# Kernel tuning notes

Measured on AMD Instinct MI355X. Metric: run time of the kernel, lower is better.

The kernel has to match this reference:

```python
import jax, jax.numpy as jnp
import numpy as np

N, L = 16, 1024
VOCAB = 32000
D_EMB = 512
D_HID = 512
N_LAYER = 2
N_CLASS = 64
NEG_INF = -1.0e9


def setup_inputs() -> dict:
    key = jax.random.key(0)
    ks = jax.random.split(key, 12)
    s = 0.02
    return {
        "x": jax.random.randint(ks[0], (N, L), 0, VOCAB),
        "eos": jax.random.randint(ks[1], (N,), 0, L),
        "emb": jax.random.normal(ks[2], (VOCAB, D_EMB), jnp.float32) * s,
        # stacked RNN weights: layer 0 input is D_EMB == D_HID so stacking is valid
        "W_ih": jax.random.normal(ks[3], (N_LAYER, D_HID, D_HID), jnp.float32) * s,
        "W_hh": jax.random.normal(ks[4], (N_LAYER, D_HID, D_HID), jnp.float32) * s,
        "b_ih": jax.random.normal(ks[5], (N_LAYER, D_HID), jnp.float32) * s,
        "b_hh": jax.random.normal(ks[6], (N_LAYER, D_HID), jnp.float32) * s,
        "Wc": jax.random.normal(ks[7], (D_HID, 2 * D_HID), jnp.float32) * s,
        "bc": jax.random.normal(ks[8], (D_HID,), jnp.float32) * s,
        "Wd": jax.random.normal(ks[9], (N_CLASS, D_HID), jnp.float32) * s,
        "bd": jax.random.normal(ks[10], (N_CLASS,), jnp.float32) * s,
    }


def _rnn(inp, W_ih, W_hh, b_ih, b_hh):
    # inp: (N, L, D); stacked tanh Elman RNN, batch_first
    out = inp
    for l in range(N_LAYER):
        Wi, Wh = W_ih[l], W_hh[l]
        b = b_ih[l] + b_hh[l]
        xs = jnp.einsum('nld,hd->lnh', out, Wi) + b  # precompute input proj, (L,N,H)
        def step(h, xt):
            h = jnp.tanh(xt + h @ Wh.T)
            return h, h
        h0 = jnp.zeros((out.shape[0], D_HID), out.dtype)
        _, ys = jax.lax.scan(step, h0, xs)  # (L, N, H)
        out = ys.transpose(1, 0, 2)
    return out


def _attention(out):
    # scores[b,t,s] = <out[b,t], out[b,s]>; strict-causal mask as in the torch code:
    # tril(scores, -1) + triu(-1e9) (diagonal and above get -1e9)
    scores = jnp.einsum('bld,bmd->blm', out, out)
    Lm = scores.shape[-1]
    masked = jnp.tril(scores, -1) + jnp.triu(jnp.full((Lm, Lm), NEG_INF, scores.dtype))
    att = jax.nn.softmax(masked, axis=-1)
    att_vec = jnp.einsum('blm,bmd->bld', att, out)
    return att_vec, att


def reference(x, eos, emb, W_ih, W_hh, b_ih, b_hh, Wc, bc, Wd, bd):
    h = emb[x]                                   # (N, L, D_EMB)
    out = _rnn(h, W_ih, W_hh, b_ih, b_hh)        # (N, L, D_HID)
    att_vec, att_scores = _attention(out)
    # one-hot(eos) matmul == gather at eos position
    idx = jnp.arange(out.shape[0])
    z = out[idx, eos]                            # (N, D_HID)
    att_z = att_vec[idx, eos]                    # (N, D_HID)
    dec_in = jnp.concatenate([att_z, z], axis=-1) @ Wc.T + bc
    logit = dec_in @ Wd.T + bd                   # (N, N_CLASS)
    return logit
```

## Files before the change

### kernel.cpp

```cpp
#include <hip/hip_runtime.h>
#include <cmath>

#define NB   16
#define LL   1024
#define DD   512
#define NCLS 64

__global__ __launch_bounds__(256) void k_gemm_embed(
    const int* __restrict__ x, const float* __restrict__ emb,
    const float* __restrict__ W, const float* __restrict__ b1,
    const float* __restrict__ b2, float* __restrict__ C)
{
  __shared__ __align__(16) float As[16][132];
  __shared__ __align__(16) float Ws[16][132];
  const int tid = threadIdx.x;
  const int n0 = (blockIdx.x & 3) * 128;
  const int m0 = (blockIdx.x >> 2) * 128;
  const int tm = tid & 15, tn = tid >> 4;
  float acc[8][8] = {};

  const int r = tid >> 1;
  const int q = (tid & 1) * 2;
  const long arow = (long)x[m0 + r] * DD;
  const long wrow = (long)(n0 + r) * DD;

  float4 a0 = *(const float4*)(emb + arow + q * 4);
  float4 a1 = *(const float4*)(emb + arow + q * 4 + 4);
  float4 w0 = *(const float4*)(W + wrow + q * 4);
  float4 w1 = *(const float4*)(W + wrow + q * 4 + 4);

  for (int k0 = 0; k0 < DD; k0 += 16) {
    __syncthreads();
    As[q*4+0][r]=a0.x; As[q*4+1][r]=a0.y; As[q*4+2][r]=a0.z; As[q*4+3][r]=a0.w;
    As[q*4+4][r]=a1.x; As[q*4+5][r]=a1.y; As[q*4+6][r]=a1.z; As[q*4+7][r]=a1.w;
    Ws[q*4+0][r]=w0.x; Ws[q*4+1][r]=w0.y; Ws[q*4+2][r]=w0.z; Ws[q*4+3][r]=w0.w;
    Ws[q*4+4][r]=w1.x; Ws[q*4+5][r]=w1.y; Ws[q*4+6][r]=w1.z; Ws[q*4+7][r]=w1.w;
    if (k0 + 16 < DD) {
      a0 = *(const float4*)(emb + arow + k0 + 16 + q * 4);
      a1 = *(const float4*)(emb + arow + k0 + 16 + q * 4 + 4);
      w0 = *(const float4*)(W + wrow + k0 + 16 + q * 4);
      w1 = *(const float4*)(W + wrow + k0 + 16 + q * 4 + 4);
    }
    __syncthreads();
    #pragma unroll
    for (int kk = 0; kk < 16; ++kk) {
      float4 aL = *(const float4*)&As[kk][tm * 4];
      float4 aH = *(const float4*)&As[kk][64 + tm * 4];
      float4 wL = *(const float4*)&Ws[kk][tn * 4];
      float4 wH = *(const float4*)&Ws[kk][64 + tn * 4];
      const float av[8] = {aL.x,aL.y,aL.z,aL.w, aH.x,aH.y,aH.z,aH.w};
      const float wv[8] = {wL.x,wL.y,wL.z,wL.w, wH.x,wH.y,wH.z,wH.w};
      #pragma unroll
      for (int i = 0; i < 8; ++i)
        #pragma unroll
        for (int j = 0; j < 8; ++j)
          acc[i][j] += av[i] * wv[j];
    }
  }
  float bj[8];
  #pragma unroll
  for (int j = 0; j < 8; ++j) {
    const int c = n0 + ((j < 4) ? tn * 4 + j : 64 + tn * 4 + (j - 4));
    bj[j] = b1[c] + b2[c];
  }
  #pragma unroll
  for (int i = 0; i < 8; ++i) {
    const int m = m0 + ((i < 4) ? tm * 4 + i : 64 + tm * 4 + (i - 4));
    float4 o1 = { acc[i][0]+bj[0], acc[i][1]+bj[1], acc[i][2]+bj[2], acc[i][3]+bj[3] };
    float4 o2 = { acc[i][4]+bj[4], acc[i][5]+bj[5], acc[i][6]+bj[6], acc[i][7]+bj[7] };
    *(float4*)(C + (long)m * DD + n0 + tn * 4)      = o1;
    *(float4*)(C + (long)m * DD + n0 + 64 + tn * 4) = o2;
  }
}

template<int CTRL>
__device__ __forceinline__ float dpp_add(float x) {
  int s = __builtin_amdgcn_update_dpp(0, __float_as_int(x), CTRL, 0xF, 0xF, true);
  return x + __int_as_float(s);
}
__device__ __forceinline__ float wave_red8(float y) {
  y = dpp_add<0xB1>(y);
  y = dpp_add<0x4E>(y);
  y = dpp_add<0x141>(y);
  return y;
}

__device__ __forceinline__ float fast_tanh(float x) {
  float e = __expf(2.0f * x);
  return 1.0f - __fdividef(2.0f, 1.0f + e);
}

__device__ __forceinline__ float poll_ld(const float* p) {
  return __hip_atomic_load(p, __ATOMIC_RELAXED, __HIP_MEMORY_SCOPE_AGENT);
}
__device__ __forceinline__ void enc_st(float* p, float v) {
  __hip_atomic_store(p, v + 2.0f, __ATOMIC_RELAXED, __HIP_MEMORY_SCOPE_AGENT);
}
__device__ __forceinline__ void st_drain() {
  asm volatile("s_waitcnt vmcnt(0)" ::: "memory");
}
__device__ __forceinline__ void dot64(const float* w, const float4* h4, float4& a) {
  #pragma unroll
  for (int q = 0; q < 16; ++q) {
    float4 h = h4[q];
    a.x += w[4*q+0]*h.x; a.y += w[4*q+1]*h.y;
    a.z += w[4*q+2]*h.z; a.w += w[4*q+3]*h.w;
  }
}
__device__ __forceinline__ float hsum4(const float4& a) { return (a.x+a.y)+(a.z+a.w); }

__global__ __launch_bounds__(256, 2) void k_scan(
    const float* __restrict__ W_ih, const float* __restrict__ W_hh,
    const float* __restrict__ b_ih, const float* __restrict__ b_hh,
    float* __restrict__ Bbuf,
    float* __restrict__ Abuf)
{
  const int g = blockIdx.x;
  const int lay = g >> 8;
  const int b = g & 15;
  const int j = (g & 255) >> 4;
  const int tid = threadIdx.x;
  const int part = tid & 7;
  const int rl  = tid >> 3;
  const int row = j * 32 + rl;
  const bool leader = (part == 0);

  __shared__ __align__(16) float hS[2][8 * 68];
  __shared__ __align__(16) float hT[2][8 * 68];

  float* Bb = Bbuf + (long)b * LL * DD;
  float* Ab = Abuf + (long)b * LL * DD;

  const int i0 = tid, i1 = tid + 256;
  const int d0 = (i0 >> 6) * 68 + (i0 & 63);
  const int d1 = (i1 >> 6) * 68 + (i1 & 63);

  if (lay == 0) {
    float w1[64];
    {
      const float* p1 = W_hh + (long)row * DD + part * 64;
      #pragma unroll
      for (int q = 0; q < 64; ++q) w1[q] = p1[q];
    }
    #pragma unroll
    for (int q = 0; q < 64; ++q) asm volatile("" : "+v"(w1[q]));

    float xpv = 0.f, xnext = 0.f;
    if (leader) {
      xpv   = Bb[row];
      xnext = Bb[DD + row];
      enc_st(Bb + row, fast_tanh(xpv));
    }
    st_drain();
    for (int t = 1; t < LL; ++t) {
      const int bufi = t & 1;
      xpv = xnext;
      if (leader && (t + 1 < LL)) xnext = Bb[(long)(t + 1) * DD + row];
      const float* s1 = Bb + (long)(t - 1) * DD;
      float v0 = poll_ld(s1 + i0), v1 = poll_ld(s1 + i1);
      while (fminf(v0, v1) <= 1.0f) {
        __builtin_amdgcn_s_sleep(2);
        v0 = poll_ld(s1 + i0); v1 = poll_ld(s1 + i1);
      }
      hS[bufi][d0] = v0 - 2.0f; hS[bufi][d1] = v1 - 2.0f;
      __syncthreads();
      float4 a = {0.f, 0.f, 0.f, 0.f};
      dot64(w1, (const float4*)&hS[bufi][part * 68], a);
      float y = wave_red8(hsum4(a));
      if (leader) enc_st(Bb + (long)t * DD + row, fast_tanh(xpv + y));
      st_drain();
    }
  } else {
    float w2[64], w3[64];
    {
      const float* p2 = W_ih + (long)DD * DD + (long)row * DD + part * 64;
      const float* p3 = W_hh + (long)DD * DD + (long)row * DD + part * 64;
      #pragma unroll
      for (int q = 0; q < 64; ++q) { w2[q] = p2[q]; w3[q] = p3[q]; }
    }
    #pragma unroll
    for (int q = 0; q < 64; ++q) {
      asm volatile("" : "+v"(w2[q]));
      asm volatile("" : "+v"(w3[q]));
    }
    const float bias2 = b_ih[DD + row] + b_hh[DD + row];

    float xin2;
    {
      const float* s1 = Bb;
      float v0 = poll_ld(s1 + i0), v1 = poll_ld(s1 + i1);
      while (fminf(v0, v1) <= 1.0f) {
        __builtin_amdgcn_s_sleep(2);
        v0 = poll_ld(s1 + i0); v1 = poll_ld(s1 + i1);
      }
      hT[1][d0] = v0 - 2.0f; hT[1][d1] = v1 - 2.0f;
      __syncthreads();
      float4 a = {0.f, 0.f, 0.f, 0.f};
      dot64(w2, (const float4*)&hT[1][part * 68], a);
      xin2 = wave_red8(hsum4(a)) + bias2;
    }
    for (int t = 0; t < LL; ++t) {
      const int bufi = t & 1;
      const bool st2 = (t >= 1);
      const bool st1 = (t + 1 < LL);
      {
        const float* s2 = Ab + (long)(t - 1) * DD;
        const float* s1 = Bb + (long)(t + 1) * DD;
        float u0 = 3.f, u1 = 3.f, v0 = 3.f, v1 = 3.f;
        if (st2) { u0 = poll_ld(s2 + i0); u1 = poll_ld(s2 + i1); }
        if (st1) { v0 = poll_ld(s1 + i0); v1 = poll_ld(s1 + i1); }
        while (fminf(fminf(u0, u1), fminf(v0, v1)) <= 1.0f) {
          __builtin_amdgcn_s_sleep(2);
          if (st2) { u0 = poll_ld(s2 + i0); u1 = poll_ld(s2 + i1); }
          if (st1) { v0 = poll_ld(s1 + i0); v1 = poll_ld(s1 + i1); }
        }
        if (st2) { hS[bufi][d0] = u0 - 2.0f; hS[bufi][d1] = u1 - 2.0f; }
        if (st1) { hT[bufi][d0] = v0 - 2.0f; hT[bufi][d1] = v1 - 2.0f; }
      }
      __syncthreads();
      float y3 = 0.f;
      if (st2) {
        float4 a = {0.f, 0.f, 0.f, 0.f};
        dot64(w3, (const float4*)&hS[bufi][part * 68], a);
        y3 = hsum4(a);
      }
      y3 = wave_red8(y3);
      if (leader) enc_st(Ab + (long)t * DD + row, fast_tanh(xin2 + y3));
      st_drain();
      if (st1) {
        float4 a = {0.f, 0.f, 0.f, 0.f};
        dot64(w2, (const float4*)&hT[bufi][part * 68], a);
        xin2 = wave_red8(hsum4(a)) + bias2;
      }
    }
  }
}

__global__ __launch_bounds__(256) void k_attn(
    const float* __restrict__ O2, const int* __restrict__ eos,
    const float* __restrict__ Wc, const float* __restrict__ bc,
    const float* __restrict__ Wd, const float* __restrict__ bd,
    float* __restrict__ out)
{
  const int b = blockIdx.x;
  const int tid = threadIdx.x;
  const int te = eos[b];
  __shared__ __align__(16) float q[DD];
  __shared__ float ps[LL];
  __shared__ float red[256];
  __shared__ __align__(16) float din[2 * DD];
  __shared__ __align__(16) float dvec[DD];
  const float* Ob = O2 + (long)b * LL * DD;
  const float4* Ob4 = (const float4*)Ob;

  float qpart = 0.f;
  for (int i = tid; i < DD; i += 256) {
    float v = Ob[(long)te * DD + i] - 2.0f;
    q[i] = v; qpart += v;
  }
  red[tid] = qpart; __syncthreads();
  for (int off = 128; off > 0; off >>= 1) {
    if (tid < off) red[tid] += red[tid + off];
    __syncthreads();
  }
  const float qsum = red[0];
  __syncthreads();
  const float4* q4 = (const float4*)q;

  for (int ss = tid; ss < LL; ss += 256) {
    float sc = -1.0e9f;
    if (ss < te) {
      float4 acc = {0.f, 0.f, 0.f, 0.f};
      for (int kq = 0; kq < 128; ++kq) {
        float4 o = Ob4[ss * 128 + kq];
        float4 qq = q4[kq];
        acc.x += o.x*qq.x; acc.y += o.y*qq.y; acc.z += o.z*qq.z; acc.w += o.w*qq.w;
      }
      sc = acc.x + acc.y + acc.z + acc.w - 2.0f * qsum;
    }
    ps[ss] = sc;
  }
  __syncthreads();
  float m = -3.0e38f;
  for (int ss = tid; ss < LL; ss += 256) m = fmaxf(m, ps[ss]);
  red[tid] = m; __syncthreads();
  for (int off = 128; off > 0; off >>= 1) {
    if (tid < off) red[tid] = fmaxf(red[tid], red[tid + off]);
    __syncthreads();
  }
  m = red[0]; __syncthreads();
  float lsum = 0.f;
  for (int ss = tid; ss < LL; ss += 256) {
    float e = expf(ps[ss] - m);
    ps[ss] = e; lsum += e;
  }
  __syncthreads();
  red[tid] = lsum; __syncthreads();
  for (int off = 128; off > 0; off >>= 1) {
    if (tid < off) red[tid] += red[tid + off];
    __syncthreads();
  }
  const float inv = 1.0f / red[0];
  __syncthreads();
  for (int ss = tid; ss < LL; ss += 256) ps[ss] *= inv;
  __syncthreads();

  if (tid < 128) {
    float4 acc = {0.f, 0.f, 0.f, 0.f};
    for (int ss = 0; ss < LL; ++ss) {
      float p = ps[ss];
      if (p != 0.0f) {
        float4 o = Ob4[ss * 128 + tid];
        acc.x += p*o.x; acc.y += p*o.y; acc.z += p*o.z; acc.w += p*o.w;
      }
    }
    acc.x -= 2.0f; acc.y -= 2.0f; acc.z -= 2.0f; acc.w -= 2.0f;
    ((float4*)din)[tid] = acc;
  } else {
    const int c = tid - 128;
    ((float4*)din)[128 + c] = q4[c];
  }
  __syncthreads();

  const float4* din4 = (const float4*)din;
  for (int jj = tid; jj < DD; jj += 256) {
    const float4* wrow = (const float4*)(Wc + (long)jj * 2 * DD);
    float4 acc = {0.f, 0.f, 0.f, 0.f};
    for (int iq = 0; iq < 256; ++iq) {
      float4 w = wrow[iq]; float4 d = din4[iq];
      acc.x += w.x*d.x; acc.y += w.y*d.y; acc.z += w.z*d.z; acc.w += w.w*d.w;
    }
    dvec[jj] = bc[jj] + acc.x + acc.y + acc.z + acc.w;
  }
  __syncthreads();

  if (tid < NCLS) {
    const float4* wrow = (const float4*)(Wd + (long)tid * DD);
    const float4* dv4 = (const float4*)dvec;
    float4 acc = {0.f, 0.f, 0.f, 0.f};
    for (int iq = 0; iq < 128; ++iq) {
      float4 w = wrow[iq]; float4 d = dv4[iq];
      acc.x += w.x*d.x; acc.y += w.y*d.y; acc.z += w.z*d.z; acc.w += w.w*d.w;
    }
    out[b * NCLS + tid] = bd[tid] + acc.x + acc.y + acc.z + acc.w;
  }
}

extern "C" void kernel_launch(void* const* d_in, const int* in_sizes, int n_in,
                              void* d_out, int out_size, void* d_ws, size_t ws_size,
                              hipStream_t stream)
{
  const int*   x    = (const int*)  d_in[0];
  const int*   eos  = (const int*)  d_in[1];
  const float* emb  = (const float*)d_in[2];
  const float* W_ih = (const float*)d_in[3];
  const float* W_hh = (const float*)d_in[4];
  const float* b_ih = (const float*)d_in[5];
  const float* b_hh = (const float*)d_in[6];
  const float* Wc   = (const float*)d_in[7];
  const float* bc   = (const float*)d_in[8];
  const float* Wd   = (const float*)d_in[9];
  const float* bd   = (const float*)d_in[10];
  float* out = (float*)d_out;

  float* Abuf = (float*)d_ws;
  float* Bbuf = Abuf + (size_t)NB * LL * DD;

  k_gemm_embed<<<512, 256, 0, stream>>>(x, emb, W_ih, b_ih, b_hh, Bbuf);
  k_scan<<<512, 256, 0, stream>>>(W_ih, W_hh, b_ih, b_hh, Bbuf, Abuf);
  k_attn<<<NB, 256, 0, stream>>>(Abuf, eos, Wc, bc, Wd, bd, out);
}
```

Baseline: 2.001 ms.

## Fuse attention and decoder head into scan kernel tail blocks

Removes the separate attention kernel launch: layer-0 block j==0 of each batch, after finishing its scan, polls for the final layer-1 output and then runs the attention, softmax and classifier head in place. Shared memory is merged into one buffer reused for both phases. Layer-1 blocks also move the store drain after the input-projection dot product so that work overlaps the outstanding store. This saves launch overhead and the kernel boundary, but it relies on a spin-wait across blocks and therefore on all blocks being co-resident.

After: 1.748 ms. -12.6%, faster.

```diff
diff --git a/kernel.cpp b/kernel.cpp
--- a/kernel.cpp
+++ b/kernel.cpp
@@ -113,7 +113,11 @@
     const float* __restrict__ W_ih, const float* __restrict__ W_hh,
     const float* __restrict__ b_ih, const float* __restrict__ b_hh,
     float* __restrict__ Bbuf,
-    float* __restrict__ Abuf)
+    float* __restrict__ Abuf,
+    const int* __restrict__ eos,
+    const float* __restrict__ Wc, const float* __restrict__ bc,
+    const float* __restrict__ Wd, const float* __restrict__ bd,
+    float* __restrict__ out)
 {
   const int g = blockIdx.x;
   const int lay = g >> 8;
@@ -125,8 +129,9 @@
   const int row = j * 32 + rl;
   const bool leader = (part == 0);
 
-  __shared__ __align__(16) float hS[2][8 * 68];
-  __shared__ __align__(16) float hT[2][8 * 68];
+  __shared__ __align__(16) float smem[3328];
+  float* hS = smem;
+  float* hT = smem + 1088;
 
   float* Bb = Bbuf + (long)b * LL * DD;
   float* Ab = Abuf + (long)b * LL * DD;
@@ -136,39 +141,152 @@
   const int d1 = (i1 >> 6) * 68 + (i1 & 63);
 
   if (lay == 0) {
-    float w1[64];
     {
-      const float* p1 = W_hh + (long)row * DD + part * 64;
+      float w1[64];
+      {
+        const float* p1 = W_hh + (long)row * DD + part * 64;
+        #pragma unroll
+        for (int q = 0; q < 64; ++q) w1[q] = p1[q];
+      }
       #pragma unroll
-      for (int q = 0; q < 64; ++q) w1[q] = p1[q];
-    }
-    #pragma unroll
-    for (int q = 0; q < 64; ++q) asm volatile("" : "+v"(w1[q]));
-
-    float xpv = 0.f, xnext = 0.f;
-    if (leader) {
-      xpv   = Bb[row];
-      xnext = Bb[DD + row];
-      enc_st(Bb + row, fast_tanh(xpv));
-    }
-    st_drain();
-    for (int t = 1; t < LL; ++t) {
-      const int bufi = t & 1;
-      xpv = xnext;
-      if (leader && (t + 1 < LL)) xnext = Bb[(long)(t + 1) * DD + row];
-      const float* s1 = Bb + (long)(t - 1) * DD;
-      float v0 = poll_ld(s1 + i0), v1 = poll_ld(s1 + i1);
+      for (int q = 0; q < 64; ++q) asm volatile("" : "+v"(w1[q]));
+
+      float xpv = 0.f, xnext = 0.f;
+      if (leader) {
+        xpv   = Bb[row];
+        xnext = Bb[DD + row];
+        enc_st(Bb + row, fast_tanh(xpv));
+      }
+      st_drain();
+      for (int t = 1; t < LL; ++t) {
+        const int bufi = t & 1;
+        xpv = xnext;
+        if (leader && (t + 1 < LL)) xnext = Bb[(long)(t + 1) * DD + row];
+        const float* s1 = Bb + (long)(t - 1) * DD;
+        float v0 = poll_ld(s1 + i0), v1 = poll_ld(s1 + i1);
+        while (fminf(v0, v1) <= 1.0f) {
+          __builtin_amdgcn_s_sleep(2);
+          v0 = poll_ld(s1 + i0); v1 = poll_ld(s1 + i1);
+        }
+        hS[bufi*544 + d0] = v0 - 2.0f; hS[bufi*544 + d1] = v1 - 2.0f;
+        __syncthreads();
+        float4 a = {0.f, 0.f, 0.f, 0.f};
+        dot64(w1, (const float4*)&hS[bufi*544 + part * 68], a);
+        float y = wave_red8(hsum4(a));
+        if (leader) enc_st(Bb + (long)t * DD + row, fast_tanh(xpv + y));
+        st_drain();
+      }
+    }
+    if (j != 0) return;
+
+    {
+      const float* fin = Ab + (long)(LL - 1) * DD;
+      float v0 = poll_ld(fin + i0), v1 = poll_ld(fin + i1);
       while (fminf(v0, v1) <= 1.0f) {
         __builtin_amdgcn_s_sleep(2);
-        v0 = poll_ld(s1 + i0); v1 = poll_ld(s1 + i1);
-      }
-      hS[bufi][d0] = v0 - 2.0f; hS[bufi][d1] = v1 - 2.0f;
-      __syncthreads();
-      float4 a = {0.f, 0.f, 0.f, 0.f};
-      dot64(w1, (const float4*)&hS[bufi][part * 68], a);
-      float y = wave_red8(hsum4(a));
-      if (leader) enc_st(Bb + (long)t * DD + row, fast_tanh(xpv + y));
-      st_drain();
+        v0 = poll_ld(fin + i0); v1 = poll_ld(fin + i1);
+      }
+    }
+    __syncthreads();
+    float* q    = smem;
+    float* ps   = smem + 512;
+    float* red  = smem + 1536;
+    float* din  = smem + 1792;
+    float* dvec = smem + 2816;
+    const int te = eos[b];
+    const float* Ob = Ab;
+    const float4* Ob4 = (const float4*)Ob;
+
+    float qpart = 0.f;
+    for (int i = tid; i < DD; i += 256) {
+      float v = poll_ld(Ob + (long)te * DD + i) - 2.0f;
+      q[i] = v; qpart += v;
+    }
+    red[tid] = qpart; __syncthreads();
+    for (int off = 128; off > 0; off >>= 1) {
+      if (tid < off) red[tid] += red[tid + off];
+      __syncthreads();
+    }
+    const float qsum = red[0];
+    __syncthreads();
+    const float4* q4 = (const float4*)q;
+
+    for (int ss = tid; ss < LL; ss += 256) {
+      float sc = -1.0e9f;
+      if (ss < te) {
+        float4 acc = {0.f, 0.f, 0.f, 0.f};
+        for (int kq = 0; kq < 128; ++kq) {
+          float4 o = Ob4[ss * 128 + kq];
+          float4 qq = q4[kq];
+          acc.x += o.x*qq.x; acc.y += o.y*qq.y; acc.z += o.z*qq.z; acc.w += o.w*qq.w;
+        }
+        sc = acc.x + acc.y + acc.z + acc.w - 2.0f * qsum;
+      }
+      ps[ss] = sc;
+    }
+    __syncthreads();
+    float m = -3.0e38f;
+    for (int ss = tid; ss < LL; ss += 256) m = fmaxf(m, ps[ss]);
+    red[tid] = m; __syncthreads();
+    for (int off = 128; off > 0; off >>= 1) {
+      if (tid < off) red[tid] = fmaxf(red[tid], red[tid + off]);
+      __syncthreads();
+    }
+    m = red[0]; __syncthreads();
+    float lsum = 0.f;
+    for (int ss = tid; ss < LL; ss += 256) {
+      float e = expf(ps[ss] - m);
+      ps[ss] = e; lsum += e;
+    }
+    __syncthreads();
+    red[tid] = lsum; __syncthreads();
+    for (int off = 128; off > 0; off >>= 1) {
+      if (tid < off) red[tid] += red[tid + off];
+      __syncthreads();
+    }
+    const float inv = 1.0f / red[0];
+    __syncthreads();
+    for (int ss = tid; ss < LL; ss += 256) ps[ss] *= inv;
+    __syncthreads();
+
+    if (tid < 128) {
+      float4 acc = {0.f, 0.f, 0.f, 0.f};
+      for (int ss = 0; ss < LL; ++ss) {
+        float p = ps[ss];
+        if (p != 0.0f) {
+          float4 o = Ob4[ss * 128 + tid];
+          acc.x += p*o.x; acc.y += p*o.y; acc.z += p*o.z; acc.w += p*o.w;
+        }
+      }
+      acc.x -= 2.0f; acc.y -= 2.0f; acc.z -= 2.0f; acc.w -= 2.0f;
+      ((float4*)din)[tid] = acc;
+    } else {
+      const int c = tid - 128;
+      ((float4*)din)[128 + c] = q4[c];
+    }
+    __syncthreads();
+
+    const float4* din4 = (const float4*)din;
+    for (int jj = tid; jj < DD; jj += 256) {
+      const float4* wrow = (const float4*)(Wc + (long)jj * 2 * DD);
+      float4 acc = {0.f, 0.f, 0.f, 0.f};
+      for (int iq = 0; iq < 256; ++iq) {
+        float4 w = wrow[iq]; float4 d = din4[iq];
+        acc.x += w.x*d.x; acc.y += w.y*d.y; acc.z += w.z*d.z; acc.w += w.w*d.w;
+      }
+      dvec[jj] = bc[jj] + acc.x + acc.y + acc.z + acc.w;
+    }
+    __syncthreads();
+
+    if (tid < NCLS) {
+      const float4* wrow = (const float4*)(Wd + (long)tid * DD);
+      const float4* dv4 = (const float4*)dvec;
+      float4 acc = {0.f, 0.f, 0.f, 0.f};
+      for (int iq = 0; iq < 128; ++iq) {
+        float4 w = wrow[iq]; float4 d = dv4[iq];
+        acc.x += w.x*d.x; acc.y += w.y*d.y; acc.z += w.z*d.z; acc.w += w.w*d.w;
+      }
+      out[b * NCLS + tid] = bd[tid] + acc.x + acc.y + acc.z + acc.w;
     }
   } else {
     float w2[64], w3[64];
@@ -193,10 +311,10 @@
         __builtin_amdgcn_s_sleep(2);
         v0 = poll_ld(s1 + i0); v1 = poll_ld(s1 + i1);
       }
-      hT[1][d0] = v0 - 2.0f; hT[1][d1] = v1 - 2.0f;
+      hT[544 + d0] = v0 - 2.0f; hT[544 + d1] = v1 - 2.0f;
       __syncthreads();
       float4 a = {0.f, 0.f, 0.f, 0.f};
-      dot64(w2, (const float4*)&hT[1][part * 68], a);
+      dot64(w2, (const float4*)&hT[544 + part * 68], a);
       xin2 = wave_red8(hsum4(a)) + bias2;
     }
     for (int t = 0; t < LL; ++t) {
@@ -214,135 +332,25 @@
           if (st2) { u0 = poll_ld(s2 + i0); u1 = poll_ld(s2 + i1); }
           if (st1) { v0 = poll_ld(s1 + i0); v1 = poll_ld(s1 + i1); }
         }
-        if (st2) { hS[bufi][d0] = u0 - 2.0f; hS[bufi][d1] = u1 - 2.0f; }
-        if (st1) { hT[bufi][d0] = v0 - 2.0f; hT[bufi][d1] = v1 - 2.0f; }
+        if (st2) { hS[bufi*544 + d0] = u0 - 2.0f; hS[bufi*544 + d1] = u1 - 2.0f; }
+        if (st1) { hT[bufi*544 + d0] = v0 - 2.0f; hT[bufi*544 + d1] = v1 - 2.0f; }
       }
       __syncthreads();
       float y3 = 0.f;
       if (st2) {
         float4 a = {0.f, 0.f, 0.f, 0.f};
-        dot64(w3, (const float4*)&hS[bufi][part * 68], a);
+        dot64(w3, (const float4*)&hS[bufi*544 + part * 68], a);
         y3 = hsum4(a);
       }
       y3 = wave_red8(y3);
       if (leader) enc_st(Ab + (long)t * DD + row, fast_tanh(xin2 + y3));
-      st_drain();
       if (st1) {
         float4 a = {0.f, 0.f, 0.f, 0.f};
-        dot64(w2, (const float4*)&hT[bufi][part * 68], a);
+        dot64(w2, (const float4*)&hT[bufi*544 + part * 68], a);
         xin2 = wave_red8(hsum4(a)) + bias2;
       }
-    }
-  }
-}
-
-__global__ __launch_bounds__(256) void k_attn(
-    const float* __restrict__ O2, const int* __restrict__ eos,
-    const float* __restrict__ Wc, const float* __restrict__ bc,
-    const float* __restrict__ Wd, const float* __restrict__ bd,
-    float* __restrict__ out)
-{
-  const int b = blockIdx.x;
-  const int tid = threadIdx.x;
-  const int te = eos[b];
-  __shared__ __align__(16) float q[DD];
-  __shared__ float ps[LL];
-  __shared__ float red[256];
-  __shared__ __align__(16) float din[2 * DD];
-  __shared__ __align__(16) float dvec[DD];
-  const float* Ob = O2 + (long)b * LL * DD;
-  const float4* Ob4 = (const float4*)Ob;
-
-  float qpart = 0.f;
-  for (int i = tid; i < DD; i += 256) {
-    float v = Ob[(long)te * DD + i] - 2.0f;
-    q[i] = v; qpart += v;
-  }
-  red[tid] = qpart; __syncthreads();
-  for (int off = 128; off > 0; off >>= 1) {
-    if (tid < off) red[tid] += red[tid + off];
-    __syncthreads();
-  }
-  const float qsum = red[0];
-  __syncthreads();
-  const float4* q4 = (const float4*)q;
-
-  for (int ss = tid; ss < LL; ss += 256) {
-    float sc = -1.0e9f;
-    if (ss < te) {
-      float4 acc = {0.f, 0.f, 0.f, 0.f};
-      for (int kq = 0; kq < 128; ++kq) {
-        float4 o = Ob4[ss * 128 + kq];
-        float4 qq = q4[kq];
-        acc.x += o.x*qq.x; acc.y += o.y*qq.y; acc.z += o.z*qq.z; acc.w += o.w*qq.w;
-      }
-      sc = acc.x + acc.y + acc.z + acc.w - 2.0f * qsum;
-    }
-    ps[ss] = sc;
-  }
-  __syncthreads();
-  float m = -3.0e38f;
-  for (int ss = tid; ss < LL; ss += 256) m = fmaxf(m, ps[ss]);
-  red[tid] = m; __syncthreads();
-  for (int off = 128; off > 0; off >>= 1) {
-    if (tid < off) red[tid] = fmaxf(red[tid], red[tid + off]);
-    __syncthreads();
-  }
-  m = red[0]; __syncthreads();
-  float lsum = 0.f;
-  for (int ss = tid; ss < LL; ss += 256) {
-    float e = expf(ps[ss] - m);
-    ps[ss] = e; lsum += e;
-  }
-  __syncthreads();
-  red[tid] = lsum; __syncthreads();
-  for (int off = 128; off > 0; off >>= 1) {
-    if (tid < off) red[tid] += red[tid + off];
-    __syncthreads();
-  }
-  const float inv = 1.0f / red[0];
-  __syncthreads();
-  for (int ss = tid; ss < LL; ss += 256) ps[ss] *= inv;
-  __syncthreads();
-
-  if (tid < 128) {
-    float4 acc = {0.f, 0.f, 0.f, 0.f};
-    for (int ss = 0; ss < LL; ++ss) {
-      float p = ps[ss];
-      if (p != 0.0f) {
-        float4 o = Ob4[ss * 128 + tid];
-        acc.x += p*o.x; acc.y += p*o.y; acc.z += p*o.z; acc.w += p*o.w;
-      }
-    }
-    acc.x -= 2.0f; acc.y -= 2.0f; acc.z -= 2.0f; acc.w -= 2.0f;
-    ((float4*)din)[tid] = acc;
-  } else {
-    const int c = tid - 128;
-    ((float4*)din)[128 + c] = q4[c];
-  }
-  __syncthreads();
-
-  const float4* din4 = (const float4*)din;
-  for (int jj = tid; jj < DD; jj += 256) {
-    const float4* wrow = (const float4*)(Wc + (long)jj * 2 * DD);
-    float4 acc = {0.f, 0.f, 0.f, 0.f};
-    for (int iq = 0; iq < 256; ++iq) {
-      float4 w = wrow[iq]; float4 d = din4[iq];
-      acc.x += w.x*d.x; acc.y += w.y*d.y; acc.z += w.z*d.z; acc.w += w.w*d.w;
-    }
-    dvec[jj] = bc[jj] + acc.x + acc.y + acc.z + acc.w;
-  }
-  __syncthreads();
-
-  if (tid < NCLS) {
-    const float4* wrow = (const float4*)(Wd + (long)tid * DD);
-    const float4* dv4 = (const float4*)dvec;
-    float4 acc = {0.f, 0.f, 0.f, 0.f};
-    for (int iq = 0; iq < 128; ++iq) {
-      float4 w = wrow[iq]; float4 d = dv4[iq];
-      acc.x += w.x*d.x; acc.y += w.y*d.y; acc.z += w.z*d.z; acc.w += w.w*d.w;
-    }
-    out[b * NCLS + tid] = bd[tid] + acc.x + acc.y + acc.z + acc.w;
+      st_drain();
+    }
   }
 }
 
@@ -367,6 +375,6 @@
   float* Bbuf = Abuf + (size_t)NB * LL * DD;
 
   k_gemm_embed<<<512, 256, 0, stream>>>(x, emb, W_ih, b_ih, b_hh, Bbuf);
-  k_scan<<<512, 256, 0, stream>>>(W_ih, W_hh, b_ih, b_hh, Bbuf, Abuf);
-  k_attn<<<NB, 256, 0, stream>>>(Abuf, eos, Wc, bc, Wd, bd, out);
-}
+  k_scan<<<512, 256, 0, stream>>>(W_ih, W_hh, b_ih, b_hh, Bbuf, Abuf,
+                                  eos, Wc, bc, Wd, bd, out);
+}
```
